# Kernel optimization log

Hardware: AMD Instinct MI355X
Metric: run time of the kernel (lower is better)

Reference implementation:

```python
import jax, jax.numpy as jnp
import numpy as np

K = 7  # g_decode_kernel_size


def _linear(x, W, b):
    # torch nn.Linear: y = x @ W.T + b, W: [out, in]
    return jnp.matmul(x, W.T) + b


def _shifted_conv(x, w, b):
    # x: [B, D, L]; causal conv: pad left K-1 (== pad both sides K-1 then trim right K-1)
    y = jax.lax.conv_general_dilated(
        x, w, window_strides=(1,), padding=[(K - 1, 0)],
        dimension_numbers=("NCH", "OIH", "NCH"))
    y = y + b[None, :, None]  # [B, 2D, L]
    D = x.shape[1]
    gated = y[:, :D, :] * jax.nn.sigmoid(y[:, D:, :])
    return gated + x


def setup_inputs() -> dict:
    key = jax.random.key(0)
    ks = jax.random.split(key, 16)
    B, T, L = 64, 64, 32
    E_enc, emb, D, A, V = 1024, 512, 512, 512, 30000

    def rn(k, shape, fan_in):
        return jax.random.normal(k, shape, dtype=jnp.float32) * (1.0 / np.sqrt(fan_in))

    return {
        "features": jax.random.normal(ks[0], (B, T, E_enc), dtype=jnp.float32),
        "captions": jax.random.randint(ks[1], (B, L), 0, V),
        "lengths": jax.random.randint(ks[2], (B,), 0, L),
        "embed_W": jax.random.normal(ks[3], (V, emb), dtype=jnp.float32) * 0.02,
        "W1": rn(ks[4], (D, emb + E_enc), emb + E_enc),
        "b1": jnp.zeros((D,), jnp.float32),
        "conv_w1": rn(ks[5], (2 * D, D, K), D * K),
        "conv_b1": jnp.zeros((2 * D,), jnp.float32),
        "conv_w2": rn(ks[6], (2 * D, D, K), D * K),
        "conv_b2": jnp.zeros((2 * D,), jnp.float32),
        "Wenc": rn(ks[7], (A, E_enc), E_enc),
        "benc": jnp.zeros((A,), jnp.float32),
        "Wdec": rn(ks[8], (A, D), D),
        "bdec": jnp.zeros((A,), jnp.float32),
        "Wp": rn(ks[9], (1, A), A),
        "bp": jnp.zeros((1,), jnp.float32),
        "W2": rn(ks[10], (V, E_enc + D), E_enc + D),
        "b2": jnp.zeros((V,), jnp.float32),
    }


def reference(features, captions, lengths, embed_W, W1, b1, conv_w1, conv_b1,
              conv_w2, conv_b2, Wenc, benc, Wdec, bdec, Wp, bp, W2, b2):
    # features: [B, T, E_enc]; captions: [B, L] int
    embeddings = embed_W[captions]                      # [B, L, emb]
    enc_mean = jnp.mean(features, axis=1, keepdims=True)  # [B, 1, E_enc]
    enc_mean = jnp.broadcast_to(enc_mean, (features.shape[0], embeddings.shape[1], features.shape[2]))
    x = jnp.concatenate([enc_mean, embeddings], axis=2)  # [B, L, E_enc+emb]
    x = _linear(x, W1, b1)                               # [B, L, D]
    x = jnp.transpose(x, (0, 2, 1))                      # [B, D, L]
    x = _shifted_conv(x, conv_w1, conv_b1)
    x = _shifted_conv(x, conv_w2, conv_b2)
    decode = jnp.transpose(x, (0, 2, 1))[:, :-1, :]      # [B, L-1, D]

    # Attention (vectorized over decode steps). NOTE: original code computes
    # tanh but discards it (assigns to misspelled 'featrues'), so NO tanh here.
    f_att = _linear(features, Wenc, benc)                # [B, T, A]
    d_att = _linear(decode, Wdec, bdec)                  # [B, S, A]
    # linear_prob applied to (f_att[:,None,t]+d_att[:,s,None]) -> scalar scores
    scores = (f_att[:, None, :, :] + d_att[:, :, None, :]) @ Wp[0] + bp[0]  # [B, S, T]
    attw = jax.nn.softmax(scores, axis=-1)               # softmax over T
    ctx = jnp.einsum("bst,bte->bse", attw, features)     # [B, S, E_enc]

    out = jnp.concatenate([ctx, decode], axis=2)         # [B, S, E_enc+D]
    logits = _linear(out, W2, b2)                        # [B, S, vocab]
    return logits
```

## Files before the change

kernel.cpp:

```cpp
#include <hip/hip_runtime.h>
#include <hip/hip_bf16.h>
#include <math.h>

#define B 64
#define T 64
#define E_ENC 1024
#define EMB 512
#define D 512
#define L 32
#define S 31
#define A 512
#define V 30000
#define KSZ 7
#define KC (D * KSZ)

typedef __attribute__((ext_vector_type(8))) short bf16x8;
typedef __attribute__((ext_vector_type(4))) float f32x4;

__device__ __forceinline__ unsigned short f2bf(float f) {
  union { float f; unsigned int u; } x; x.f = f;
  unsigned int r = (x.u + 0x7fffu + ((x.u >> 16) & 1u)) >> 16;
  return (unsigned short)r;
}

__device__ __forceinline__ void gload_lds16(const void* g, void* l) {
  __builtin_amdgcn_global_load_lds(
      (const __attribute__((address_space(1))) unsigned int*)g,
      (__attribute__((address_space(3))) unsigned int*)l, 16, 0, 0);
}

__global__ void k_wv(const float* __restrict__ Wenc, const float* __restrict__ Wp,
                     const float* __restrict__ benc, float* __restrict__ wv,
                     float* __restrict__ c0) {
  __shared__ float red[256];
  int e = blockIdx.x * 256 + threadIdx.x;
  float s = 0.f;
  for (int a = 0; a < A; ++a) s += Wp[a] * Wenc[(size_t)a * E_ENC + e];
  wv[e] = s;
  if (blockIdx.x == 0) {
    int t = threadIdx.x;
    float v = Wp[t] * benc[t] + Wp[t + 256] * benc[t + 256];
    red[t] = v;
    __syncthreads();
    for (int off = 128; off > 0; off >>= 1) {
      if (t < off) red[t] += red[t + off];
      __syncthreads();
    }
    if (t == 0) c0[0] = red[0];
  }
}

__global__ void k_mean_ctx(const float* __restrict__ features, const float* __restrict__ wv,
                           const float* __restrict__ c0, unsigned short* __restrict__ enc_meanb,
                           unsigned short* __restrict__ ctxb) {
  int b = blockIdx.x, tid = threadIdx.x;
  const float* fb = features + (size_t)b * T * E_ENC;
  __shared__ float s_attw[T];

  float m0 = 0, m1 = 0, m2 = 0, m3 = 0;
  for (int t = 0; t < T; ++t) {
    const float* r = fb + t * E_ENC;
    m0 += r[tid]; m1 += r[tid + 256]; m2 += r[tid + 512]; m3 += r[tid + 768];
  }
  size_t eb = (size_t)b * E_ENC;
  enc_meanb[eb + tid]       = f2bf(m0 * (1.f / 64.f));
  enc_meanb[eb + tid + 256] = f2bf(m1 * (1.f / 64.f));
  enc_meanb[eb + tid + 512] = f2bf(m2 * (1.f / 64.f));
  enc_meanb[eb + tid + 768] = f2bf(m3 * (1.f / 64.f));

  {
    int t = tid >> 2, part = tid & 3;
    const float* r = fb + t * E_ENC + part * 256;
    const float* wp = wv + part * 256;
    float s = 0.f;
    for (int e = 0; e < 256; e += 4) {
      float4 f4 = *(const float4*)(r + e);
      float4 w4 = *(const float4*)(wp + e);
      s += f4.x * w4.x + f4.y * w4.y + f4.z * w4.z + f4.w * w4.w;
    }
    s += __shfl_xor(s, 1);
    s += __shfl_xor(s, 2);
    if (part == 0) s_attw[t] = s + c0[0];
  }
  __syncthreads();
  if (tid < 64) {
    float v = s_attw[tid];
    float mx = v;
    #pragma unroll
    for (int off = 32; off > 0; off >>= 1) mx = fmaxf(mx, __shfl_xor(mx, off));
    float e = expf(v - mx);
    float sm = e;
    #pragma unroll
    for (int off = 32; off > 0; off >>= 1) sm += __shfl_xor(sm, off);
    s_attw[tid] = e / sm;
  }
  __syncthreads();
  float ca = 0, cb = 0, cc = 0, cd = 0;
  for (int t = 0; t < T; ++t) {
    float w = s_attw[t];
    const float* r = fb + t * E_ENC;
    ca += w * r[tid]; cb += w * r[tid + 256]; cc += w * r[tid + 512]; cd += w * r[tid + 768];
  }
  ctxb[eb + tid]       = f2bf(ca);
  ctxb[eb + tid + 256] = f2bf(cb);
  ctxb[eb + tid + 512] = f2bf(cc);
  ctxb[eb + tid + 768] = f2bf(cd);
}

__global__ void k_gather_emb(const float* __restrict__ embed_W,
                             const int* __restrict__ captions,
                             unsigned short* __restrict__ Xe) {
  int g = blockIdx.x, tid = threadIdx.x;
  int cap = captions[g];
  const float* src = embed_W + (size_t)cap * EMB;
  float2 v = *(const float2*)(src + tid * 2);
  unsigned int pk = (unsigned int)f2bf(v.x) | ((unsigned int)f2bf(v.y) << 16);
  *(unsigned int*)(Xe + (size_t)g * EMB + tid * 2) = pk;
}

__global__ void k_cvt_w1(const float* __restrict__ W1, unsigned short* __restrict__ w1b) {
  int d = blockIdx.x, tid = threadIdx.x;
  #pragma unroll
  for (int i = 0; i < 3; ++i) {
    int c = tid * 2 + i * 512;
    float2 v = *(const float2*)(W1 + (size_t)d * (E_ENC + EMB) + c);
    unsigned int pk = (unsigned int)f2bf(v.x) | ((unsigned int)f2bf(v.y) << 16);
    *(unsigned int*)(w1b + (size_t)d * (E_ENC + EMB) + c) = pk;
  }
}

__global__ __launch_bounds__(256) void k_x1f_mfma(
    const unsigned short* __restrict__ enc_meanb,
    const unsigned short* __restrict__ Xe,
    const unsigned short* __restrict__ w1b,
    const float* __restrict__ b1, float* __restrict__ x1) {
  __shared__ __align__(16) unsigned short As[64 * 64];
  __shared__ __align__(16) unsigned short Bs[64 * 64];
  int c0 = blockIdx.x * 64, g0 = blockIdx.y * 64;
  int tid = threadIdx.x, lane = tid & 63, wave = tid >> 6;
  int wr = wave >> 1, wc = wave & 1;
  int rsel = lane & 15, hi = lane >> 4;

  f32x4 acc[2][2];
  #pragma unroll
  for (int m = 0; m < 2; ++m)
    #pragma unroll
    for (int n = 0; n < 2; ++n) acc[m][n] = (f32x4){0.f, 0.f, 0.f, 0.f};

  int r1 = tid >> 3, s1 = tid & 7;
  int sw = (s1 ^ (r1 & 7)) * 8;
  const unsigned short* emA1 = enc_meanb + (size_t)(g0 >> 5) * 1024 + sw;
  const unsigned short* emA2 = enc_meanb + (size_t)((g0 >> 5) + 1) * 1024 + sw;
  const unsigned short* xeA1 = Xe + (size_t)(g0 + r1) * 512 + sw;
  const unsigned short* xeA2 = Xe + (size_t)(g0 + r1 + 32) * 512 + sw;
  const unsigned short* gB1 = w1b + (size_t)(c0 + r1) * (E_ENC + EMB) + sw;
  const unsigned short* gB2 = w1b + (size_t)(c0 + r1 + 32) * (E_ENC + EMB) + sw;
  unsigned short* aD1 = As + wave * 512;
  unsigned short* aD2 = As + 2048 + wave * 512;
  unsigned short* bD1 = Bs + wave * 512;
  unsigned short* bD2 = Bs + 2048 + wave * 512;

  int slot0 = hi ^ (rsel & 7);
  int slot1 = (4 + hi) ^ (rsel & 7);

  for (int kt = 0; kt < 24; ++kt) {
    const unsigned short *pA1, *pA2;
    if (kt < 16) { pA1 = emA1 + kt * 64; pA2 = emA2 + kt * 64; }
    else         { pA1 = xeA1 + (kt - 16) * 64; pA2 = xeA2 + (kt - 16) * 64; }
    gload_lds16(pA1, aD1);
    gload_lds16(pA2, aD2);
    gload_lds16(gB1, bD1);
    gload_lds16(gB2, bD2);
    gB1 += 64; gB2 += 64;
    __syncthreads();

    bf16x8 af[2][2], bfr[2][2];
    #pragma unroll
    for (int m = 0; m < 2; ++m) {
      int rowA = (wr * 32 + m * 16 + rsel) * 64;
      af[m][0] = *(const bf16x8*)(As + rowA + slot0 * 8);
      af[m][1] = *(const bf16x8*)(As + rowA + slot1 * 8);
    }
    #pragma unroll
    for (int n = 0; n < 2; ++n) {
      int rowB = (wc * 32 + n * 16 + rsel) * 64;
      bfr[n][0] = *(const bf16x8*)(Bs + rowB + slot0 * 8);
      bfr[n][1] = *(const bf16x8*)(Bs + rowB + slot1 * 8);
    }
    #pragma unroll
    for (int m = 0; m < 2; ++m)
      #pragma unroll
      for (int n = 0; n < 2; ++n) {
        acc[m][n] = __builtin_amdgcn_mfma_f32_16x16x32_bf16(af[m][0], bfr[n][0], acc[m][n], 0, 0, 0);
        acc[m][n] = __builtin_amdgcn_mfma_f32_16x16x32_bf16(af[m][1], bfr[n][1], acc[m][n], 0, 0, 0);
      }
    __syncthreads();
  }

  float bvv[2];
  #pragma unroll
  for (int n = 0; n < 2; ++n) bvv[n] = b1[c0 + wc * 32 + n * 16 + rsel];
  #pragma unroll
  for (int m = 0; m < 2; ++m)
    #pragma unroll
    for (int i = 0; i < 4; ++i) {
      int g = g0 + wr * 32 + m * 16 + hi * 4 + i;
      float* xr = x1 + (size_t)g * D;
      #pragma unroll
      for (int n = 0; n < 2; ++n) {
        int c = c0 + wc * 32 + n * 16 + rsel;
        xr[c] = acc[m][n][i] + bvv[n];
      }
    }
}

__global__ void k_im2col(const float* __restrict__ x, unsigned short* __restrict__ Xc) {
  int g = blockIdx.x, tid = threadIdx.x;
  int b = g >> 5, l = g & 31;
  unsigned short* row = Xc + (size_t)g * KC;
  const float* xb = x + (size_t)b * L * D;
  int d = tid * 2;
  #pragma unroll
  for (int k = 0; k < KSZ; ++k) {
    int lp = l + k - 6;
    unsigned int pk = 0;
    if (lp >= 0) {
      float2 v = *(const float2*)(xb + (size_t)lp * D + d);
      pk = (unsigned int)f2bf(v.x) | ((unsigned int)f2bf(v.y) << 16);
    }
    *(unsigned int*)(row + k * 512 + d) = pk;
  }
}

__global__ void k_cvt_wconv(const float* __restrict__ w, unsigned short* __restrict__ wb) {
  __shared__ float row[KC];
  int c = blockIdx.x, tid = threadIdx.x;
  const float* wr = w + (size_t)c * KC;
  for (int i = tid; i < KC; i += 256) row[i] = wr[i];
  __syncthreads();
  unsigned short* ob = wb + (size_t)c * KC;
  int dp = tid * 2;
  #pragma unroll
  for (int k = 0; k < KSZ; ++k) {
    unsigned int pk = (unsigned int)f2bf(row[dp * 7 + k]) |
                      ((unsigned int)f2bf(row[(dp + 1) * 7 + k]) << 16);
    *(unsigned int*)(ob + k * 512 + dp) = pk;
  }
}

__global__ __launch_bounds__(256) void k_conv_mfma(
    const unsigned short* __restrict__ Xc, const unsigned short* __restrict__ wb,
    const float* __restrict__ bias, float* __restrict__ y) {
  __shared__ __align__(16) unsigned short As[2][64 * 64];
  __shared__ __align__(16) unsigned short Bs[2][64 * 64];
  int c0 = blockIdx.x * 64, g0 = blockIdx.y * 64;
  int tid = threadIdx.x, lane = tid & 63, wave = tid >> 6;
  int wr = wave >> 1, wc = wave & 1;
  int rsel = lane & 15, hi = lane >> 4;

  f32x4 acc[2][2];
  #pragma unroll
  for (int m = 0; m < 2; ++m)
    #pragma unroll
    for (int n = 0; n < 2; ++n) acc[m][n] = (f32x4){0.f, 0.f, 0.f, 0.f};

  int r1 = tid >> 3, s1 = tid & 7;
  int sw = (s1 ^ (r1 & 7)) * 8;
  const unsigned short* gA1 = Xc + (size_t)(g0 + r1) * KC + sw;
  const unsigned short* gA2 = Xc + (size_t)(g0 + r1 + 32) * KC + sw;
  const unsigned short* gB1 = wb + (size_t)(c0 + r1) * KC + sw;
  const unsigned short* gB2 = wb + (size_t)(c0 + r1 + 32) * KC + sw;

  int slot0 = hi ^ (rsel & 7);
  int slot1 = (4 + hi) ^ (rsel & 7);

  gload_lds16(gA1, &As[0][wave * 512]);
  gload_lds16(gA2, &As[0][2048 + wave * 512]);
  gload_lds16(gB1, &Bs[0][wave * 512]);
  gload_lds16(gB2, &Bs[0][2048 + wave * 512]);
  gA1 += 64; gA2 += 64; gB1 += 64; gB2 += 64;
  __syncthreads();

  int cur = 0;
  for (int kt = 0; kt < KC / 64; ++kt) {
    if (kt + 1 < KC / 64) {
      int nb = cur ^ 1;
      gload_lds16(gA1, &As[nb][wave * 512]);
      gload_lds16(gA2, &As[nb][2048 + wave * 512]);
      gload_lds16(gB1, &Bs[nb][wave * 512]);
      gload_lds16(gB2, &Bs[nb][2048 + wave * 512]);
      gA1 += 64; gA2 += 64; gB1 += 64; gB2 += 64;
    }

    bf16x8 af[2][2], bfr[2][2];
    #pragma unroll
    for (int m = 0; m < 2; ++m) {
      int rowA = (wr * 32 + m * 16 + rsel) * 64;
      af[m][0] = *(const bf16x8*)(&As[cur][rowA + slot0 * 8]);
      af[m][1] = *(const bf16x8*)(&As[cur][rowA + slot1 * 8]);
    }
    #pragma unroll
    for (int n = 0; n < 2; ++n) {
      int rowB = (wc * 32 + n * 16 + rsel) * 64;
      bfr[n][0] = *(const bf16x8*)(&Bs[cur][rowB + slot0 * 8]);
      bfr[n][1] = *(const bf16x8*)(&Bs[cur][rowB + slot1 * 8]);
    }
    #pragma unroll
    for (int m = 0; m < 2; ++m)
      #pragma unroll
      for (int n = 0; n < 2; ++n) {
        acc[m][n] = __builtin_amdgcn_mfma_f32_16x16x32_bf16(af[m][0], bfr[n][0], acc[m][n], 0, 0, 0);
        acc[m][n] = __builtin_amdgcn_mfma_f32_16x16x32_bf16(af[m][1], bfr[n][1], acc[m][n], 0, 0, 0);
      }
    __syncthreads();
    cur ^= 1;
  }

  float bv[2];
  #pragma unroll
  for (int n = 0; n < 2; ++n) bv[n] = bias[c0 + wc * 32 + n * 16 + rsel];
  #pragma unroll
  for (int m = 0; m < 2; ++m)
    #pragma unroll
    for (int i = 0; i < 4; ++i) {
      int g = g0 + wr * 32 + m * 16 + hi * 4 + i;
      float* yr = y + (size_t)g * 1024;
      #pragma unroll
      for (int n = 0; n < 2; ++n)
        yr[c0 + wc * 32 + n * 16 + rsel] = acc[m][n][i] + bv[n];
    }
}

__global__ void k_glu(const float* __restrict__ y, const float* __restrict__ xres,
                      float* __restrict__ xout) {
  int idx = blockIdx.x * 256 + threadIdx.x;
  int g = idx >> 7, d4 = (idx & 127) << 2;
  const float* yr = y + (size_t)g * 1024;
  float4 a = *(const float4*)(yr + d4);
  float4 bq = *(const float4*)(yr + 512 + d4);
  float4 xr = *(const float4*)(xres + (size_t)g * 512 + d4);
  float4 o;
  o.x = a.x / (1.f + expf(-bq.x)) + xr.x;
  o.y = a.y / (1.f + expf(-bq.y)) + xr.y;
  o.z = a.z / (1.f + expf(-bq.z)) + xr.z;
  o.w = a.w / (1.f + expf(-bq.w)) + xr.w;
  *(float4*)(xout + (size_t)g * 512 + d4) = o;
}

__global__ void k_glu_bf16(const float* __restrict__ y, const float* __restrict__ xres,
                           unsigned short* __restrict__ xout) {
  int idx = blockIdx.x * 256 + threadIdx.x;
  int g = idx >> 7, d4 = (idx & 127) << 2;
  const float* yr = y + (size_t)g * 1024;
  float4 a = *(const float4*)(yr + d4);
  float4 bq = *(const float4*)(yr + 512 + d4);
  float4 xr = *(const float4*)(xres + (size_t)g * 512 + d4);
  ushort4 o;
  o.x = f2bf(a.x / (1.f + expf(-bq.x)) + xr.x);
  o.y = f2bf(a.y / (1.f + expf(-bq.y)) + xr.y);
  o.z = f2bf(a.z / (1.f + expf(-bq.z)) + xr.z);
  o.w = f2bf(a.w / (1.f + expf(-bq.w)) + xr.w);
  *(ushort4*)(xout + (size_t)g * 512 + d4) = o;
}

__global__ __launch_bounds__(256) void k_cbase_mfma(
    const unsigned short* __restrict__ ctxb,
    const float* __restrict__ W2,
    const float* __restrict__ b2, float* __restrict__ cbase) {
  __shared__ __align__(16) unsigned short As[64 * 64];
  __shared__ __align__(16) unsigned short Bs[128 * 64];
  int v0 = blockIdx.x * 128;
  int tid = threadIdx.x, lane = tid & 63, wave = tid >> 6;
  int rsel = lane & 15, hi = lane >> 4;
  int wc = wave;

  f32x4 acc[4][2];
  #pragma unroll
  for (int m = 0; m < 4; ++m)
    #pragma unroll
    for (int n = 0; n < 2; ++n) acc[m][n] = (f32x4){0.f, 0.f, 0.f, 0.f};

  int ra1 = tid >> 3, sa = tid & 7;
  int ra2 = ra1 + 32;
  const unsigned short* gA1 = ctxb + (size_t)ra1 * 1024 + (sa ^ (ra1 & 7)) * 8;
  const unsigned short* gA2 = ctxb + (size_t)ra2 * 1024 + (sa ^ (ra2 & 7)) * 8;
  unsigned short* aD1 = As + wave * 512;
  unsigned short* aD2 = As + 2048 + wave * 512;

  const float* gB[4];
  int bofs[4];
  #pragma unroll
  for (int p = 0; p < 4; ++p) {
    int row = p * 32 + (tid >> 3);
    int seg = tid & 7;
    int vr = v0 + row; if (vr > V - 1) vr = V - 1;
    gB[p] = W2 + (size_t)vr * (E_ENC + D) + seg * 8;
    bofs[p] = row * 64 + (seg ^ (row & 7)) * 8;
  }

  for (int kt = 0; kt < 16; ++kt) {
    gload_lds16(gA1, aD1);
    gload_lds16(gA2, aD2);
    gA1 += 64; gA2 += 64;
    #pragma unroll
    for (int p = 0; p < 4; ++p) {
      float4 f0 = *(const float4*)(gB[p]);
      float4 f1 = *(const float4*)(gB[p] + 4);
      gB[p] += 64;
      bf16x8 o;
      o[0] = (short)f2bf(f0.x); o[1] = (short)f2bf(f0.y);
      o[2] = (short)f2bf(f0.z); o[3] = (short)f2bf(f0.w);
      o[4] = (short)f2bf(f1.x); o[5] = (short)f2bf(f1.y);
      o[6] = (short)f2bf(f1.z); o[7] = (short)f2bf(f1.w);
      *(bf16x8*)(Bs + bofs[p]) = o;
    }
    __syncthreads();

    bf16x8 af[4][2], bfr[2][2];
    #pragma unroll
    for (int m = 0; m < 4; ++m) {
      int rowA = (m * 16 + rsel) * 64;
      #pragma unroll
      for (int kk = 0; kk < 2; ++kk)
        af[m][kk] = *(const bf16x8*)(As + rowA + ((kk * 4 + hi) ^ (rsel & 7)) * 8);
    }
    #pragma unroll
    for (int n = 0; n < 2; ++n) {
      int rowB = (wc * 32 + n * 16 + rsel) * 64;
      #pragma unroll
      for (int kk = 0; kk < 2; ++kk)
        bfr[n][kk] = *(const bf16x8*)(Bs + rowB + ((kk * 4 + hi) ^ (rsel & 7)) * 8);
    }
    #pragma unroll
    for (int kk = 0; kk < 2; ++kk)
      #pragma unroll
      for (int m = 0; m < 4; ++m)
        #pragma unroll
        for (int n = 0; n < 2; ++n)
          acc[m][n] = __builtin_amdgcn_mfma_f32_16x16x32_bf16(af[m][kk], bfr[n][kk], acc[m][n], 0, 0, 0);
    __syncthreads();
  }

  #pragma unroll
  for (int n = 0; n < 2; ++n) {
    int v = v0 + wc * 32 + n * 16 + rsel;
    if (v >= V) continue;
    float bias = b2[v];
    #pragma unroll
    for (int m = 0; m < 4; ++m)
      #pragma unroll
      for (int i = 0; i < 4; ++i) {
        int b = m * 16 + hi * 4 + i;
        cbase[(size_t)b * V + v] = acc[m][n][i] + bias;
      }
  }
}

__global__ void k_cvt_w2d(const float* __restrict__ W2, unsigned short* __restrict__ y) {
  int i = blockIdx.x * 256 + threadIdx.x;
  int row = i >> 7, c = (i & 127) << 2;
  float4 f = *(const float4*)(W2 + (size_t)row * (E_ENC + D) + E_ENC + c);
  ushort4 o;
  o.x = f2bf(f.x); o.y = f2bf(f.y); o.z = f2bf(f.z); o.w = f2bf(f.w);
  *(ushort4*)(y + (size_t)row * D + c) = o;
}

__global__ __launch_bounds__(256) void k_logits_mfma(
    const unsigned short* __restrict__ Ab,
    const unsigned short* __restrict__ Bb,
    const float* __restrict__ cbase, float* __restrict__ out) {
  __shared__ __align__(16) unsigned short As[2][128 * 32];
  __shared__ __align__(16) unsigned short Bs[2][128 * 32];
  int flat = blockIdx.x;
  int ord = (flat & 7) * 470 + (flat >> 3);
  int v0 = (ord >> 4) * 128, g0 = (ord & 15) * 128;
  int tid = threadIdx.x, lane = tid & 63, wave = tid >> 6;
  int wr = wave >> 1, wc = wave & 1;
  int rsel = lane & 15, hi = lane >> 4;

  f32x4 acc[4][4];
  #pragma unroll
  for (int m = 0; m < 4; ++m)
    #pragma unroll
    for (int n = 0; n < 4; ++n) acc[m][n] = (f32x4){0.f, 0.f, 0.f, 0.f};

  int r1 = tid >> 2, s1 = tid & 3;
  int seg = (s1 ^ ((r1 >> 1) & 3)) * 8;
  const unsigned short* gA1 = Ab + (size_t)(g0 + r1) * 512 + seg;
  const unsigned short* gA2 = Ab + (size_t)(g0 + r1 + 64) * 512 + seg;
  int vr1 = v0 + r1;      if (vr1 > V - 1) vr1 = V - 1;
  int vr2 = v0 + r1 + 64; if (vr2 > V - 1) vr2 = V - 1;
  const unsigned short* gB1 = Bb + (size_t)vr1 * 512 + seg;
  const unsigned short* gB2 = Bb + (size_t)vr2 * 512 + seg;

  gload_lds16(gA1, &As[0][wave * 512]);
  gload_lds16(gA2, &As[0][2048 + wave * 512]);
  gload_lds16(gB1, &Bs[0][wave * 512]);
  gload_lds16(gB2, &Bs[0][2048 + wave * 512]);
  gA1 += 32; gA2 += 32; gB1 += 32; gB2 += 32;
  __syncthreads();

  int sl = (rsel >> 1) & 3;
  int cur = 0;
  for (int kt = 0; kt < 16; ++kt) {
    if (kt + 1 < 16) {
      int nb = cur ^ 1;
      gload_lds16(gA1, &As[nb][wave * 512]);
      gload_lds16(gA2, &As[nb][2048 + wave * 512]);
      gload_lds16(gB1, &Bs[nb][wave * 512]);
      gload_lds16(gB2, &Bs[nb][2048 + wave * 512]);
      gA1 += 32; gA2 += 32; gB1 += 32; gB2 += 32;
    }

    bf16x8 af[4], bfr[4];
    #pragma unroll
    for (int m = 0; m < 4; ++m)
      af[m] = *(const bf16x8*)(&As[cur][(wr * 64 + m * 16 + rsel) * 32 + ((hi ^ sl) * 8)]);
    #pragma unroll
    for (int n = 0; n < 4; ++n)
      bfr[n] = *(const bf16x8*)(&Bs[cur][(wc * 64 + n * 16 + rsel) * 32 + ((hi ^ sl) * 8)]);
    #pragma unroll
    for (int m = 0; m < 4; ++m)
      #pragma unroll
      for (int n = 0; n < 4; ++n)
        acc[m][n] = __builtin_amdgcn_mfma_f32_16x16x32_bf16(af[m], bfr[n], acc[m][n], 0, 0, 0);
    __syncthreads();
    cur ^= 1;
  }

  #pragma unroll
  for (int m = 0; m < 4; ++m) {
    #pragma unroll
    for (int i = 0; i < 4; ++i) {
      int g = g0 + wr * 64 + m * 16 + hi * 4 + i;
      int b = g >> 5, lt = g & 31;
      if (lt >= S) continue;
      size_t orow = ((size_t)b * S + lt) * V;
      const float* cb = cbase + (size_t)b * V;
      #pragma unroll
      for (int n = 0; n < 4; ++n) {
        int v = v0 + wc * 64 + n * 16 + rsel;
        if (v < V) out[orow + v] = acc[m][n][i] + cb[v];
      }
    }
  }
}

extern "C" void kernel_launch(void* const* d_in, const int* in_sizes, int n_in,
                              void* d_out, int out_size, void* d_ws, size_t ws_size,
                              hipStream_t stream) {
  const float* features = (const float*)d_in[0];
  const int*   captions = (const int*)d_in[1];
  const float* embed_W  = (const float*)d_in[3];
  const float* W1   = (const float*)d_in[4];
  const float* b1   = (const float*)d_in[5];
  const float* cw1  = (const float*)d_in[6];
  const float* cb1  = (const float*)d_in[7];
  const float* cw2  = (const float*)d_in[8];
  const float* cb2  = (const float*)d_in[9];
  const float* Wenc = (const float*)d_in[10];
  const float* benc = (const float*)d_in[11];
  const float* Wp   = (const float*)d_in[14];
  const float* W2   = (const float*)d_in[16];
  const float* b2   = (const float*)d_in[17];
  float* out = (float*)d_out;

  float* ws = (float*)d_ws;
  float* wv       = ws;
  float* c0       = ws + 1024;
  unsigned short* enc_meanb = (unsigned short*)(ws + 1040);
  unsigned short* ctxb = (unsigned short*)(ws + 66576);
  float* xA       = ws + 164880;
  float* xB       = ws + 1213456;
  float* y        = ws + 2262032;
  float* cbase    = y;
  unsigned short* x3b  = (unsigned short*)xA;
  unsigned short* Xc   = (unsigned short*)(ws + 4359184);
  unsigned short* wbuf = (unsigned short*)(ws + 8029200);
  unsigned short* W2d  = (unsigned short*)(ws + 9864208);
  unsigned short* Xe  = Xc;
  unsigned short* w1b = Xc + 1048576;

  hipLaunchKernelGGL(k_cvt_w2d,  dim3(15000),   dim3(256), 0, stream, W2, W2d);
  hipLaunchKernelGGL(k_wv,       dim3(4),       dim3(256), 0, stream, Wenc, Wp, benc, wv, c0);
  hipLaunchKernelGGL(k_mean_ctx, dim3(B),       dim3(256), 0, stream, features, wv, c0, enc_meanb, ctxb);

  hipLaunchKernelGGL(k_gather_emb, dim3(2048),  dim3(256), 0, stream, embed_W, captions, Xe);
  hipLaunchKernelGGL(k_cvt_w1,     dim3(512),   dim3(256), 0, stream, W1, w1b);
  hipLaunchKernelGGL(k_x1f_mfma,   dim3(8, 32), dim3(256), 0, stream, enc_meanb, Xe, w1b, b1, xA);

  hipLaunchKernelGGL(k_cvt_wconv, dim3(1024),   dim3(256), 0, stream, cw1, wbuf);
  hipLaunchKernelGGL(k_im2col,    dim3(2048),   dim3(256), 0, stream, xA, Xc);
  hipLaunchKernelGGL(k_conv_mfma, dim3(16, 32), dim3(256), 0, stream, Xc, wbuf, cb1, y);
  hipLaunchKernelGGL(k_glu,       dim3(1024),   dim3(256), 0, stream, y, xA, xB);

  hipLaunchKernelGGL(k_cvt_wconv, dim3(1024),   dim3(256), 0, stream, cw2, wbuf);
  hipLaunchKernelGGL(k_im2col,    dim3(2048),   dim3(256), 0, stream, xB, Xc);
  hipLaunchKernelGGL(k_conv_mfma, dim3(16, 32), dim3(256), 0, stream, Xc, wbuf, cb2, y);
  hipLaunchKernelGGL(k_glu_bf16,  dim3(1024),   dim3(256), 0, stream, y, xB, x3b);

  hipLaunchKernelGGL(k_cbase_mfma, dim3(235),   dim3(256), 0, stream, ctxb, W2, b2, cbase);
  hipLaunchKernelGGL(k_logits_mfma, dim3(3760), dim3(256), 0, stream, x3b, W2d, cbase, out);
}
```

Baseline: 407.4 us.

## Fuse GLU into conv GEMM epilogue and stage logits stores through LDS

The conv GEMM now computes matching 32-column slices of both GLU halves in one block. The gate half is passed through shared memory so the sigmoid gating and residual add happen in the epilogue, which removes the separate GLU kernels and the fp32 y round trip. The logits kernel epilogue now stages accumulators in LDS and writes coalesced float4 stores with vectorized cbase loads, instead of scattered scalar stores. The cost is extra LDS syncs in both epilogues, and the float4 path assumes V-aligned column tails.

After: 370.5 us. -9.1%, faster.

```diff
diff --git a/kernel.cpp b/kernel.cpp
--- a/kernel.cpp
+++ b/kernel.cpp
@@ -248,12 +248,15 @@
   }
 }
 
-__global__ __launch_bounds__(256) void k_conv_mfma(
+template <int OUT_BF16>
+__global__ __launch_bounds__(256) void k_conv_glu(
     const unsigned short* __restrict__ Xc, const unsigned short* __restrict__ wb,
-    const float* __restrict__ bias, float* __restrict__ y) {
-  __shared__ __align__(16) unsigned short As[2][64 * 64];
-  __shared__ __align__(16) unsigned short Bs[2][64 * 64];
-  int c0 = blockIdx.x * 64, g0 = blockIdx.y * 64;
+    const float* __restrict__ bias, const float* __restrict__ xres,
+    float* __restrict__ outf, unsigned short* __restrict__ outh) {
+  __shared__ __align__(16) unsigned char csmem[32768];
+  unsigned short (*As)[64 * 64] = (unsigned short (*)[64 * 64])csmem;
+  unsigned short (*Bs)[64 * 64] = (unsigned short (*)[64 * 64])(csmem + 16384);
+  int c0 = blockIdx.x * 32, g0 = blockIdx.y * 64;
   int tid = threadIdx.x, lane = tid & 63, wave = tid >> 6;
   int wr = wave >> 1, wc = wave & 1;
   int rsel = lane & 15, hi = lane >> 4;
@@ -269,7 +272,7 @@
   const unsigned short* gA1 = Xc + (size_t)(g0 + r1) * KC + sw;
   const unsigned short* gA2 = Xc + (size_t)(g0 + r1 + 32) * KC + sw;
   const unsigned short* gB1 = wb + (size_t)(c0 + r1) * KC + sw;
-  const unsigned short* gB2 = wb + (size_t)(c0 + r1 + 32) * KC + sw;
+  const unsigned short* gB2 = wb + (size_t)(512 + c0 + r1) * KC + sw;
 
   int slot0 = hi ^ (rsel & 7);
   int slot1 = (4 + hi) ^ (rsel & 7);
@@ -316,51 +319,42 @@
     cur ^= 1;
   }
 
-  float bv[2];
-  #pragma unroll
-  for (int n = 0; n < 2; ++n) bv[n] = bias[c0 + wc * 32 + n * 16 + rsel];
-  #pragma unroll
-  for (int m = 0; m < 2; ++m)
-    #pragma unroll
-    for (int i = 0; i < 4; ++i) {
-      int g = g0 + wr * 32 + m * 16 + hi * 4 + i;
-      float* yr = y + (size_t)g * 1024;
-      #pragma unroll
-      for (int n = 0; n < 2; ++n)
-        yr[c0 + wc * 32 + n * 16 + rsel] = acc[m][n][i] + bv[n];
-    }
-}
-
-__global__ void k_glu(const float* __restrict__ y, const float* __restrict__ xres,
-                      float* __restrict__ xout) {
-  int idx = blockIdx.x * 256 + threadIdx.x;
-  int g = idx >> 7, d4 = (idx & 127) << 2;
-  const float* yr = y + (size_t)g * 1024;
-  float4 a = *(const float4*)(yr + d4);
-  float4 bq = *(const float4*)(yr + 512 + d4);
-  float4 xr = *(const float4*)(xres + (size_t)g * 512 + d4);
-  float4 o;
-  o.x = a.x / (1.f + expf(-bq.x)) + xr.x;
-  o.y = a.y / (1.f + expf(-bq.y)) + xr.y;
-  o.z = a.z / (1.f + expf(-bq.z)) + xr.z;
-  o.w = a.w / (1.f + expf(-bq.w)) + xr.w;
-  *(float4*)(xout + (size_t)g * 512 + d4) = o;
-}
-
-__global__ void k_glu_bf16(const float* __restrict__ y, const float* __restrict__ xres,
-                           unsigned short* __restrict__ xout) {
-  int idx = blockIdx.x * 256 + threadIdx.x;
-  int g = idx >> 7, d4 = (idx & 127) << 2;
-  const float* yr = y + (size_t)g * 1024;
-  float4 a = *(const float4*)(yr + d4);
-  float4 bq = *(const float4*)(yr + 512 + d4);
-  float4 xr = *(const float4*)(xres + (size_t)g * 512 + d4);
-  ushort4 o;
-  o.x = f2bf(a.x / (1.f + expf(-bq.x)) + xr.x);
-  o.y = f2bf(a.y / (1.f + expf(-bq.y)) + xr.y);
-  o.z = f2bf(a.z / (1.f + expf(-bq.z)) + xr.z);
-  o.w = f2bf(a.w / (1.f + expf(-bq.w)) + xr.w);
-  *(ushort4*)(xout + (size_t)g * 512 + d4) = o;
+  float* sb = (float*)csmem;
+  float bvv[2];
+  #pragma unroll
+  for (int n = 0; n < 2; ++n)
+    bvv[n] = wc ? bias[512 + c0 + n * 16 + rsel] : bias[c0 + n * 16 + rsel];
+  if (wc) {
+    #pragma unroll
+    for (int m = 0; m < 2; ++m)
+      #pragma unroll
+      for (int i = 0; i < 4; ++i) {
+        int lr = wr * 32 + m * 16 + hi * 4 + i;
+        #pragma unroll
+        for (int n = 0; n < 2; ++n)
+          sb[lr * 33 + n * 16 + rsel] = acc[m][n][i] + bvv[n];
+      }
+  }
+  __syncthreads();
+  if (!wc) {
+    #pragma unroll
+    for (int m = 0; m < 2; ++m)
+      #pragma unroll
+      for (int i = 0; i < 4; ++i) {
+        int lr = wr * 32 + m * 16 + hi * 4 + i;
+        int g = g0 + lr;
+        const float* xr = xres + (size_t)g * 512 + c0;
+        #pragma unroll
+        for (int n = 0; n < 2; ++n) {
+          int d = n * 16 + rsel;
+          float ya = acc[m][n][i] + bvv[n];
+          float yb = sb[lr * 33 + d];
+          float val = ya / (1.f + expf(-yb)) + xr[d];
+          if (OUT_BF16) outh[(size_t)g * 512 + c0 + d] = f2bf(val);
+          else          outf[(size_t)g * 512 + c0 + d] = val;
+        }
+      }
+  }
 }
 
 __global__ __launch_bounds__(256) void k_cbase_mfma(
@@ -469,8 +463,9 @@
     const unsigned short* __restrict__ Ab,
     const unsigned short* __restrict__ Bb,
     const float* __restrict__ cbase, float* __restrict__ out) {
-  __shared__ __align__(16) unsigned short As[2][128 * 32];
-  __shared__ __align__(16) unsigned short Bs[2][128 * 32];
+  __shared__ __align__(16) unsigned char smem[33792];
+  unsigned short (*As)[128 * 32] = (unsigned short (*)[128 * 32])smem;
+  unsigned short (*Bs)[128 * 32] = (unsigned short (*)[128 * 32])(smem + 16384);
   int flat = blockIdx.x;
   int ord = (flat & 7) * 470 + (flat >> 3);
   int v0 = (ord >> 4) * 128, g0 = (ord & 15) * 128;
@@ -528,19 +523,36 @@
     cur ^= 1;
   }
 
-  #pragma unroll
-  for (int m = 0; m < 4; ++m) {
-    #pragma unroll
-    for (int i = 0; i < 4; ++i) {
-      int g = g0 + wr * 64 + m * 16 + hi * 4 + i;
+  float* ebuf = (float*)smem;
+  #pragma unroll
+  for (int h = 0; h < 2; ++h) {
+    if (h) __syncthreads();
+    if (wr == h) {
+      #pragma unroll
+      for (int m = 0; m < 4; ++m)
+        #pragma unroll
+        for (int i = 0; i < 4; ++i) {
+          int lr = m * 16 + hi * 4 + i;
+          #pragma unroll
+          for (int n = 0; n < 4; ++n)
+            ebuf[lr * 132 + wc * 64 + n * 16 + rsel] = acc[m][n][i];
+        }
+    }
+    __syncthreads();
+    #pragma unroll
+    for (int j = 0; j < 8; ++j) {
+      int f = tid + j * 256;
+      int lr = f >> 5, c4 = (f & 31) * 4;
+      int g = g0 + h * 64 + lr;
       int b = g >> 5, lt = g & 31;
-      if (lt >= S) continue;
-      size_t orow = ((size_t)b * S + lt) * V;
-      const float* cb = cbase + (size_t)b * V;
-      #pragma unroll
-      for (int n = 0; n < 4; ++n) {
-        int v = v0 + wc * 64 + n * 16 + rsel;
-        if (v < V) out[orow + v] = acc[m][n][i] + cb[v];
+      int v = v0 + c4;
+      if (lt < S && v < V) {
+        float4 val = *(const float4*)(ebuf + lr * 132 + c4);
+        float4 cb4 = *(const float4*)(cbase + (size_t)b * V + v);
+        float4 o;
+        o.x = val.x + cb4.x; o.y = val.y + cb4.y;
+        o.z = val.z + cb4.z; o.w = val.w + cb4.w;
+        *(float4*)(out + ((size_t)b * S + lt) * V + v) = o;
       }
     }
   }
@@ -572,8 +584,7 @@
   unsigned short* ctxb = (unsigned short*)(ws + 66576);
   float* xA       = ws + 164880;
   float* xB       = ws + 1213456;
-  float* y        = ws + 2262032;
-  float* cbase    = y;
+  float* cbase    = ws + 2262032;
   unsigned short* x3b  = (unsigned short*)xA;
   unsigned short* Xc   = (unsigned short*)(ws + 4359184);
   unsigned short* wbuf = (unsigned short*)(ws + 8029200);
@@ -589,15 +600,13 @@
   hipLaunchKernelGGL(k_cvt_w1,     dim3(512),   dim3(256), 0, stream, W1, w1b);
   hipLaunchKernelGGL(k_x1f_mfma,   dim3(8, 32), dim3(256), 0, stream, enc_meanb, Xe, w1b, b1, xA);
 
-  hipLaunchKernelGGL(k_cvt_wconv, dim3(1024),   dim3(256), 0, stream, cw1, wbuf);
-  hipLaunchKernelGGL(k_im2col,    dim3(2048),   dim3(256), 0, stream, xA, Xc);
-  hipLaunchKernelGGL(k_conv_mfma, dim3(16, 32), dim3(256), 0, stream, Xc, wbuf, cb1, y);
-  hipLaunchKernelGGL(k_glu,       dim3(1024),   dim3(256), 0, stream, y, xA, xB);
-
-  hipLaunchKernelGGL(k_cvt_wconv, dim3(1024),   dim3(256), 0, stream, cw2, wbuf);
-  hipLaunchKernelGGL(k_im2col,    dim3(2048),   dim3(256), 0, stream, xB, Xc);
-  hipLaunchKernelGGL(k_conv_mfma, dim3(16, 32), dim3(256), 0, stream, Xc, wbuf, cb2, y);
-  hipLaunchKernelGGL(k_glu_bf16,  dim3(1024),   dim3(256), 0, stream, y, xB, x3b);
+  hipLaunchKernelGGL(k_cvt_wconv,   dim3(1024),   dim3(256), 0, stream, cw1, wbuf);
+  hipLaunchKernelGGL(k_im2col,      dim3(2048),   dim3(256), 0, stream, xA, Xc);
+  hipLaunchKernelGGL(k_conv_glu<0>, dim3(16, 32), dim3(256), 0, stream, Xc, wbuf, cb1, xA, xB, (unsigned short*)nullptr);
+
+  hipLaunchKernelGGL(k_cvt_wconv,   dim3(1024),   dim3(256), 0, stream, cw2, wbuf);
+  hipLaunchKernelGGL(k_im2col,      dim3(2048),   dim3(256), 0, stream, xB, Xc);
+  hipLaunchKernelGGL(k_conv_glu<1>, dim3(16, 32), dim3(256), 0, stream, Xc, wbuf, cb2, xB, (float*)nullptr, x3b);
 
   hipLaunchKernelGGL(k_cbase_mfma, dim3(235),   dim3(256), 0, stream, ctxb, W2, b2, cbase);
   hipLaunchKernelGGL(k_logits_mfma, dim3(3760), dim3(256), 0, stream, x3b, W2d, cbase, out);
```
